# Optimization experiments

Hardware: AMD Instinct MI355X
Metric: run time of the kernel (lower is better)

Reference implementation:

```python
import jax, jax.numpy as jnp
import numpy as np
from jax.scipy.special import logsumexp

EPS = 1e-6
SINKHORN_ITERS = 8
TEMPERATURE = 1.0


def sinkhorn(logits):
    # log(clamp(t, min=eps)) / temperature, then alternating row/col log-normalization
    t = jnp.log(jnp.clip(logits, EPS)) / TEMPERATURE
    for _ in range(SINKHORN_ITERS):
        t = t - logsumexp(t, axis=-2, keepdims=True)  # over tokens n
        t = t - logsumexp(t, axis=-1, keepdims=True)  # over experts e
    return jnp.exp(t)


def setup_inputs() -> dict:
    key = jax.random.key(0)
    k1, k2, k3 = jax.random.split(key, 3)
    b, n, d, e, h = 4, 4096, 1024, 8, 1
    x = jax.random.normal(k1, (b, n, d), dtype=jnp.float32)
    gate_w = jax.random.normal(k2, (h, d, e), dtype=jnp.float32)  # to_gate_weight
    experts = jax.random.normal(k3, (e, d, d), dtype=jnp.float32) * 0.02  # expert weight tensor [e, i, o]
    return {"x": x, "gate_w": gate_w, "experts": experts}


def reference(x, gate_w, experts):
    b, n, d = x.shape
    h, _, e = gate_w.shape
    m = n // e  # tokens_per_expert

    xh = x[:, None]  # b 1 n d  (single-headed path)

    # gate logits: b h n e
    gate_logits = jnp.einsum('bhnd,hde->bhne', xh, gate_w)

    # competitive sinkhorn gates (eval mode, no gumbel noise)
    gates = sinkhorn(gate_logits)

    # topk over token dim (dim=-2) with k = tokens_per_expert
    g = jnp.swapaxes(gates, -1, -2)          # b h e n
    gv, idx = jax.lax.top_k(g, m)            # b h e m
    gate_values = jnp.swapaxes(gv, -1, -2)   # b h m e
    routed_indices = jnp.swapaxes(idx, -1, -2)  # b h m e

    # eval + competitive -> hard gates
    hard_gates = (gate_values > 0.5).astype(x.dtype)  # b h m e

    # gather routed tokens: routed[b,h,m,e,d] = x[b,h,idx[b,h,m,e],d]
    bi = jnp.arange(b)[:, None, None, None]
    hi = jnp.arange(h)[None, :, None, None]
    routed = xh[bi, hi, routed_indices]  # b h m e d

    # per-expert GEMM, vectorized over experts: experts [e,i,o] -> [e,h,i,o]
    experts4 = experts[:, None, :, :]
    out = jnp.einsum('bhmei,ehio->bhmeo', routed, experts4)  # b h m e o

    # weight by gates
    out = out * hard_gates[..., None]

    # scatter back (set semantics, as in einx set_at)
    y = jnp.zeros_like(xh).at[bi, hi, routed_indices].set(out)  # b h n d
    return y[:, 0]  # b n d
```

## Files before the change

### kernel.cpp

```cpp
#include <hip/hip_runtime.h>
#include <hip/hip_bf16.h>
#include <stdint.h>

#define BB 4
#define NN 4096
#define DD 1024
#define EE 8
#define MM 512
#define BN (BB*NN)

#define SBLK 32
#define SPB  8
#define SROWS 512

#define FRONT_GATE 512
#define FRONT_CONV 2048
#define FRONT_INIT 64
#define FRONT_BLKS (FRONT_GATE + FRONT_CONV + FRONT_INIT)

typedef __bf16 bf16x8 __attribute__((ext_vector_type(8)));
typedef float  floatx4 __attribute__((ext_vector_type(4)));

typedef const __attribute__((address_space(1))) void* gptr_t;
typedef __attribute__((address_space(3))) void* lptr_t;

__device__ __forceinline__ unsigned short f2bf(float f) {
    union { float f; unsigned u; } v; v.f = f;
    unsigned r = v.u + 0x7fffu + ((v.u >> 16) & 1u);
    return (unsigned short)(r >> 16);
}

__device__ __forceinline__ float gate_reduce8(const float acc[8], int lane) {
    float k1[4];
#pragma unroll
    for (int e = 0; e < 4; e++) {
        float a = acc[e]     + __shfl_xor(acc[e],     1, 64);
        float b = acc[e + 4] + __shfl_xor(acc[e + 4], 1, 64);
        k1[e] = (lane & 1) ? b : a;
    }
    float k2[2];
#pragma unroll
    for (int e = 0; e < 2; e++) {
        float a = k1[e]     + __shfl_xor(k1[e],     2, 64);
        float b = k1[e + 2] + __shfl_xor(k1[e + 2], 2, 64);
        k2[e] = (lane & 2) ? b : a;
    }
    float a = k2[0] + __shfl_xor(k2[0], 4, 64);
    float b = k2[1] + __shfl_xor(k2[1], 4, 64);
    float v = (lane & 4) ? b : a;
    v += __shfl_xor(v, 8, 64);
    v += __shfl_xor(v, 16, 64);
    v += __shfl_xor(v, 32, 64);
    return v;
}

#define OFF_GATES   0u
#define OFF_TOPK    524288u
#define OFF_WIN     589824u
#define OFF_COUNTS  655360u
#define OFF_LISTS   655616u
#define OFF_FLAGS   721152u
#define OFF_PART    737536u
#define OFF_KEYS    753920u
#define OFF_XBF     1802496u
#define OFF_EXPT    35356928u
#define WS_NEEDED   52134144u

__global__ __launch_bounds__(256, 2) void front_kernel(const float* __restrict__ x,
                                                       const float* __restrict__ gw,
                                                       const float* __restrict__ E,
                                                       float* __restrict__ tmat,
                                                       unsigned short* __restrict__ xbf,
                                                       unsigned short* __restrict__ expt,
                                                       int* __restrict__ win,
                                                       int* __restrict__ counts,
                                                       unsigned* __restrict__ flags) {
    __shared__ float tile[64][65];
    int bid = blockIdx.x;
    int tid = threadIdx.x;

    if (bid < FRONT_GATE) {
        int wave = tid >> 6, lane = tid & 63;
        float4 g0[4][4], g1[4][4];
#pragma unroll
        for (int j = 0; j < 4; j++)
#pragma unroll
            for (int r = 0; r < 4; r++) {
                const float4* p = (const float4*)(gw + (size_t)(j * 256 + lane * 4 + r) * 8);
                g0[j][r] = p[0];
                g1[j][r] = p[1];
            }
        int tok0 = (bid * 4 + wave) * 8;
        int exp_id = ((lane & 1) << 2) | (lane & 2) | ((lane & 4) >> 2);
        for (int tt = 0; tt < 8; tt += 2) {
            int tokA = tok0 + tt, tokB = tokA + 1;
            const float4* xrA = (const float4*)(x + (size_t)tokA * DD);
            const float4* xrB = (const float4*)(x + (size_t)tokB * DD);
            float4 xa[4], xc[4];
#pragma unroll
            for (int j = 0; j < 4; j++) xa[j] = xrA[j * 64 + lane];
#pragma unroll
            for (int j = 0; j < 4; j++) xc[j] = xrB[j * 64 + lane];
            if (xbf) {
#pragma unroll
                for (int j = 0; j < 4; j++) {
                    ushort4 o;
                    o.x = f2bf(xa[j].x); o.y = f2bf(xa[j].y); o.z = f2bf(xa[j].z); o.w = f2bf(xa[j].w);
                    ((ushort4*)(xbf + (size_t)tokA * DD))[j * 64 + lane] = o;
                }
#pragma unroll
                for (int j = 0; j < 4; j++) {
                    ushort4 o;
                    o.x = f2bf(xc[j].x); o.y = f2bf(xc[j].y); o.z = f2bf(xc[j].z); o.w = f2bf(xc[j].w);
                    ((ushort4*)(xbf + (size_t)tokB * DD))[j * 64 + lane] = o;
                }
            }
            float accA[8] = {0.f, 0.f, 0.f, 0.f, 0.f, 0.f, 0.f, 0.f};
            float accB[8] = {0.f, 0.f, 0.f, 0.f, 0.f, 0.f, 0.f, 0.f};
#pragma unroll
            for (int j = 0; j < 4; j++) {
                accA[0] += xa[j].x * g0[j][0].x + xa[j].y * g0[j][1].x + xa[j].z * g0[j][2].x + xa[j].w * g0[j][3].x;
                accA[1] += xa[j].x * g0[j][0].y + xa[j].y * g0[j][1].y + xa[j].z * g0[j][2].y + xa[j].w * g0[j][3].y;
                accA[2] += xa[j].x * g0[j][0].z + xa[j].y * g0[j][1].z + xa[j].z * g0[j][2].z + xa[j].w * g0[j][3].z;
                accA[3] += xa[j].x * g0[j][0].w + xa[j].y * g0[j][1].w + xa[j].z * g0[j][2].w + xa[j].w * g0[j][3].w;
                accA[4] += xa[j].x * g1[j][0].x + xa[j].y * g1[j][1].x + xa[j].z * g1[j][2].x + xa[j].w * g1[j][3].x;
                accA[5] += xa[j].x * g1[j][0].y + xa[j].y * g1[j][1].y + xa[j].z * g1[j][2].y + xa[j].w * g1[j][3].y;
                accA[6] += xa[j].x * g1[j][0].z + xa[j].y * g1[j][1].z + xa[j].z * g1[j][2].z + xa[j].w * g1[j][3].z;
                accA[7] += xa[j].x * g1[j][0].w + xa[j].y * g1[j][1].w + xa[j].z * g1[j][2].w + xa[j].w * g1[j][3].w;
                accB[0] += xc[j].x * g0[j][0].x + xc[j].y * g0[j][1].x + xc[j].z * g0[j][2].x + xc[j].w * g0[j][3].x;
                accB[1] += xc[j].x * g0[j][0].y + xc[j].y * g0[j][1].y + xc[j].z * g0[j][2].y + xc[j].w * g0[j][3].y;
                accB[2] += xc[j].x * g0[j][0].z + xc[j].y * g0[j][1].z + xc[j].z * g0[j][2].z + xc[j].w * g0[j][3].z;
                accB[3] += xc[j].x * g0[j][0].w + xc[j].y * g0[j][1].w + xc[j].z * g0[j][2].w + xc[j].w * g0[j][3].w;
                accB[4] += xc[j].x * g1[j][0].x + xc[j].y * g1[j][1].x + xc[j].z * g1[j][2].x + xc[j].w * g1[j][3].x;
                accB[5] += xc[j].x * g1[j][0].y + xc[j].y * g1[j][1].y + xc[j].z * g1[j][2].y + xc[j].w * g1[j][3].y;
                accB[6] += xc[j].x * g1[j][0].z + xc[j].y * g1[j][1].z + xc[j].z * g1[j][2].z + xc[j].w * g1[j][3].z;
                accB[7] += xc[j].x * g1[j][0].w + xc[j].y * g1[j][1].w + xc[j].z * g1[j][2].w + xc[j].w * g1[j][3].w;
            }
            float vA = gate_reduce8(accA, lane);
            float vB = gate_reduce8(accB, lane);
            if (lane < 8) {
                tmat[(size_t)tokA * EE + exp_id] = logf(fmaxf(vA, 1e-6f));
                tmat[(size_t)tokB * EE + exp_id] = logf(fmaxf(vB, 1e-6f));
            }
        }
    } else if (bid < FRONT_GATE + FRONT_CONV) {
        if (!expt) return;
        int cb = bid - FRONT_GATE;
        int e = cb >> 8, t = cb & 255;
        int k0 = (t >> 4) * 64, c0 = (t & 15) * 64;
#pragma unroll
        for (int ii = 0; ii < 4; ii++) {
            int r = (tid >> 4) + ii * 16;
            int c4 = (tid & 15) * 4;
            float4 v = *(const float4*)(E + ((size_t)e * DD + k0 + r) * DD + c0 + c4);
            tile[r][c4 + 0] = v.x; tile[r][c4 + 1] = v.y; tile[r][c4 + 2] = v.z; tile[r][c4 + 3] = v.w;
        }
        __syncthreads();
        int cc = tid >> 2, kk0 = (tid & 3) * 16;
#pragma unroll
        for (int q = 0; q < 4; q++) {
            ushort4 o;
            o.x = f2bf(tile[kk0 + q * 4 + 0][cc]);
            o.y = f2bf(tile[kk0 + q * 4 + 1][cc]);
            o.z = f2bf(tile[kk0 + q * 4 + 2][cc]);
            o.w = f2bf(tile[kk0 + q * 4 + 3][cc]);
            *(ushort4*)&expt[((size_t)e * DD + c0 + cc) * DD + k0 + kk0 + q * 4] = o;
        }
    } else {
        int i = (bid - FRONT_GATE - FRONT_CONV) * 256 + tid;
        win[i] = -1;
        if (i < 32) counts[i] = 0;
        if (i < 4096) flags[i] = 0u;
    }
}

__global__ __launch_bounds__(512) void sinkhorn_mb(const float* __restrict__ tmat,
                                                   float* __restrict__ part,
                                                   unsigned* __restrict__ flags,
                                                   unsigned long long* __restrict__ keys) {
    int g = blockIdx.x;
    int b = g >> 3, sl = g & 7;
    int tid = threadIdx.x;
    int wave = tid >> 6, lane = tid & 63;
    int row = sl * SROWS + tid;
    const float* tr = tmat + ((size_t)b * NN + row) * EE;
    float tv[EE];
#pragma unroll
    for (int e = 0; e < EE; e++) tv[e] = tr[e];

    __shared__ float red[8][8];
    __shared__ float bcm[8];

    for (int it = 0; it < 8; it++) {
#pragma unroll
        for (int e = 0; e < EE; e++) {
            float s = expf(tv[e]);
            for (int off = 32; off > 0; off >>= 1) s += __shfl_down(s, off, 64);
            if (lane == 0) red[wave][e] = s;
        }
        __syncthreads();
        if (tid == 0) {
            float* pm = part + (size_t)(it * 32 + b * 8 + sl) * 16;
#pragma unroll
            for (int e = 0; e < EE; e++) {
                float s = 0.f;
#pragma unroll
                for (int w = 0; w < 8; w++) s += red[w][e];
                __hip_atomic_store(&pm[e], s, __ATOMIC_RELAXED, __HIP_MEMORY_SCOPE_AGENT);
            }
            __hip_atomic_store(&flags[(size_t)(it * 32 + b * 8 + sl) * 16], 1u,
                               __ATOMIC_RELEASE, __HIP_MEMORY_SCOPE_AGENT);
        }
        if (tid < 8) {
            const unsigned* f = flags + (size_t)(it * 32 + b * 8 + tid) * 16;
            while (__hip_atomic_load(f, __ATOMIC_ACQUIRE, __HIP_MEMORY_SCOPE_AGENT) == 0u)
                __builtin_amdgcn_s_sleep(1);
        }
        __syncthreads();
        if (tid < 8) {
            const float* pb = part + (size_t)(it * 32 + b * 8) * 16;
            float s = 0.f;
#pragma unroll
            for (int p = 0; p < SPB; p++)
                s += __hip_atomic_load(&pb[p * 16 + tid], __ATOMIC_RELAXED, __HIP_MEMORY_SCOPE_AGENT);
            bcm[tid] = logf(s);
        }
        __syncthreads();
#pragma unroll
        for (int e = 0; e < EE; e++) tv[e] -= bcm[e];
        {
            float s = 0.f;
#pragma unroll
            for (int e = 0; e < EE; e++) s += expf(tv[e]);
            float lse = logf(s);
#pragma unroll
            for (int e = 0; e < EE; e++) tv[e] -= lse;
        }
    }
#pragma unroll
    for (int e = 0; e < EE; e++) {
        unsigned fb = __float_as_uint(expf(tv[e]));
        keys[(size_t)(b * EE + e) * NN + row] =
            ((unsigned long long)fb << 32) | (unsigned)(~row);
    }
}

__global__ __launch_bounds__(256) void rank_topk_kernel(const unsigned long long* __restrict__ keys,
                                                        float* __restrict__ topk_val,
                                                        int* __restrict__ win) {
    __shared__ unsigned long long K[NN];
    int be = blockIdx.y;
    int b = be >> 3, e = be & 7;
    int tid = threadIdx.x;
    const unsigned long long* kcol = keys + (size_t)be * NN;
    for (int i = tid; i < NN / 2; i += 256)
        ((ulonglong2*)K)[i] = ((const ulonglong2*)kcol)[i];
    __syncthreads();
    int t = blockIdx.x * 256 + tid;
    unsigned long long my = K[t];
    int cnt = 0;
    for (int j = 0; j < NN; j += 8) {
        ulonglong2 a = *(const ulonglong2*)&K[j + 0];
        ulonglong2 c = *(const ulonglong2*)&K[j + 2];
        ulonglong2 d = *(const ulonglong2*)&K[j + 4];
        ulonglong2 f = *(const ulonglong2*)&K[j + 6];
        cnt += (int)(a.x > my) + (int)(a.y > my) + (int)(c.x > my) + (int)(c.y > my)
             + (int)(d.x > my) + (int)(d.y > my) + (int)(f.x > my) + (int)(f.y > my);
    }
    if (cnt < MM) {
        topk_val[be * MM + cnt] = __uint_as_float((unsigned)(my >> 32));
        atomicMax(&win[b * NN + t], cnt * 8 + e);
    }
}

__global__ __launch_bounds__(256) void build_zero_kernel(const float* __restrict__ topk_val,
                                                         const int* __restrict__ win,
                                                         int* __restrict__ counts,
                                                         int* __restrict__ lists,
                                                         float* __restrict__ y) {
    __shared__ int act_s[64];
    int base = blockIdx.x * 64;
    int tid = threadIdx.x;
    if (tid < 64) {
        int i = base + tid;
        int b = i >> 12, tok = i & 4095;
        int w = win[i];
        int active = 0;
        if (w >= 0) {
            int m = w >> 3, e = w & 7;
            float gv = topk_val[(b * 8 + e) * MM + m];
            if (gv > 0.5f) {
                int p = atomicAdd(&counts[b * 8 + e], 1);
                lists[(b * 8 + e) * MM + p] = tok;
                active = 1;
            }
        }
        act_s[tid] = active;
    }
    __syncthreads();
    float4 z = make_float4(0.f, 0.f, 0.f, 0.f);
    for (int r = 0; r < 64; r++) {
        if (!act_s[r])
            ((float4*)(y + (size_t)(base + r) * DD))[tid] = z;
    }
}

__global__ __launch_bounds__(256) void expert_gemm_mfma(const unsigned short* __restrict__ xbf,
                                                        const unsigned short* __restrict__ expt,
                                                        const int* __restrict__ counts,
                                                        const int* __restrict__ lists,
                                                        float* __restrict__ y) {
    int be = blockIdx.z;
    int b = be >> 3, e = be & 7;
    int cnt = counts[be];
    int row0 = blockIdx.y * 64;
    if (row0 >= cnt) return;
    int col0 = blockIdx.x * 128;

    __shared__ unsigned short As[64 * 32];
    __shared__ unsigned short Bs[128 * 32];
    __shared__ int toks[64];

    int tid = threadIdx.x;
    int wave = tid >> 6, lane = tid & 63;
    int m16 = lane & 15, quad = lane >> 4;
    int wave_m = wave >> 1, wave_n = wave & 1;

    if (tid < 64) {
        int r = row0 + tid;
        toks[tid] = lists[be * MM + (r < cnt ? r : cnt - 1)];
    }

    int r0 = tid >> 2;
    int ch = tid & 3;

    const unsigned short* xb = xbf + (size_t)b * NN * DD;
    const unsigned short* Eb = expt + (size_t)e * DD * DD;

    floatx4 acc[2][4];
#pragma unroll
    for (int i = 0; i < 2; i++)
#pragma unroll
        for (int j = 0; j < 4; j++) acc[i][j] = (floatx4)0.f;

    for (int k0 = 0; k0 < DD; k0 += 32) {
        __syncthreads();
        {
            const unsigned short* gA  = xb + (size_t)toks[r0] * DD + k0 + ch * 8;
            const unsigned short* gB0 = Eb + (size_t)(col0 + r0) * DD + k0 + ch * 8;
            const unsigned short* gB1 = Eb + (size_t)(col0 + 64 + r0) * DD + k0 + ch * 8;
            __builtin_amdgcn_global_load_lds((gptr_t)gA,  (lptr_t)(As + (size_t)tid * 8), 16, 0, 0);
            __builtin_amdgcn_global_load_lds((gptr_t)gB0, (lptr_t)(Bs + (size_t)tid * 8), 16, 0, 0);
            __builtin_amdgcn_global_load_lds((gptr_t)gB1, (lptr_t)(Bs + 64 * 32 + (size_t)tid * 8), 16, 0, 0);
        }
        __syncthreads();
        bf16x8 af[2], bfr[4];
#pragma unroll
        for (int i = 0; i < 2; i++)
            af[i] = *(const bf16x8*)&As[(wave_m * 32 + i * 16 + m16) * 32 + quad * 8];
#pragma unroll
        for (int j = 0; j < 4; j++)
            bfr[j] = *(const bf16x8*)&Bs[(wave_n * 64 + j * 16 + m16) * 32 + quad * 8];
#pragma unroll
        for (int i = 0; i < 2; i++)
#pragma unroll
            for (int j = 0; j < 4; j++)
                acc[i][j] = __builtin_amdgcn_mfma_f32_16x16x32_bf16(af[i], bfr[j], acc[i][j], 0, 0, 0);
    }

#pragma unroll
    for (int i = 0; i < 2; i++) {
#pragma unroll
        for (int r = 0; r < 4; r++) {
            int lr = wave_m * 32 + i * 16 + quad * 4 + r;
            if (row0 + lr < cnt) {
                int tok = toks[lr];
                float* yr = y + ((size_t)b * NN + tok) * DD + col0 + wave_n * 64 + m16;
#pragma unroll
                for (int j = 0; j < 4; j++) yr[j * 16] = acc[i][j][r];
            }
        }
    }
}

__global__ __launch_bounds__(256) void expert_gemm_kernel(const float* __restrict__ x,
                                                          const float* __restrict__ experts,
                                                          const int* __restrict__ counts,
                                                          const int* __restrict__ lists,
                                                          float* __restrict__ y) {
    int be = blockIdx.z;
    int b = be >> 3, e = be & 7;
    int cnt = counts[be];
    int row0 = blockIdx.y * 64;
    if (row0 >= cnt) return;
    int col0 = blockIdx.x * 64;
    __shared__ float As2[16][68];
    __shared__ float Bs2[16][68];
    __shared__ int toks[64];
    int tid = threadIdx.x;
    if (tid < 64) {
        int r = row0 + tid;
        toks[tid] = (r < cnt) ? lists[be * MM + r] : -1;
    }
    __syncthreads();
    int tx = tid & 15, ty = tid >> 4;
    int ar = tid >> 2;
    int ak = (tid & 3) * 4;
    int bk = tid >> 4;
    int bc4 = (tid & 15) * 4;
    int atok = toks[ar];
    const float* xb = x + (size_t)b * NN * DD;
    const float* Eb = experts + (size_t)e * DD * DD + col0;
    float acc[4][4] = {};
    for (int k0 = 0; k0 < DD; k0 += 16) {
        float4 av;
        if (atok >= 0) av = *(const float4*)(xb + (size_t)atok * DD + k0 + ak);
        else av = make_float4(0.f, 0.f, 0.f, 0.f);
        float4 bv = *(const float4*)(Eb + (size_t)(k0 + bk) * DD + bc4);
        __syncthreads();
        As2[ak + 0][ar] = av.x; As2[ak + 1][ar] = av.y; As2[ak + 2][ar] = av.z; As2[ak + 3][ar] = av.w;
        *(float4*)&Bs2[bk][bc4] = bv;
        __syncthreads();
#pragma unroll
        for (int kk = 0; kk < 16; kk++) {
            float4 a = *(const float4*)&As2[kk][ty * 4];
            float4 bb = *(const float4*)&Bs2[kk][tx * 4];
            acc[0][0] += a.x * bb.x; acc[0][1] += a.x * bb.y; acc[0][2] += a.x * bb.z; acc[0][3] += a.x * bb.w;
            acc[1][0] += a.y * bb.x; acc[1][1] += a.y * bb.y; acc[1][2] += a.y * bb.z; acc[1][3] += a.y * bb.w;
            acc[2][0] += a.z * bb.x; acc[2][1] += a.z * bb.y; acc[2][2] += a.z * bb.z; acc[2][3] += a.z * bb.w;
            acc[3][0] += a.w * bb.x; acc[3][1] += a.w * bb.y; acc[3][2] += a.w * bb.z; acc[3][3] += a.w * bb.w;
        }
    }
#pragma unroll
    for (int i = 0; i < 4; i++) {
        int rl = ty * 4 + i;
        if (row0 + rl < cnt) {
            int tok = toks[rl];
            float4 o = make_float4(acc[i][0], acc[i][1], acc[i][2], acc[i][3]);
            *(float4*)(y + ((size_t)b * NN + tok) * DD + col0 + tx * 4) = o;
        }
    }
}

extern "C" void kernel_launch(void* const* d_in, const int* in_sizes, int n_in,
                              void* d_out, int out_size, void* d_ws, size_t ws_size,
                              hipStream_t stream) {
    const float* x       = (const float*)d_in[0];
    const float* gw      = (const float*)d_in[1];
    const float* experts = (const float*)d_in[2];
    float* y = (float*)d_out;

    char* ws = (char*)d_ws;
    float*    gates    = (float*)(ws + OFF_GATES);
    float*    topk_val = (float*)(ws + OFF_TOPK);
    int*      win      = (int*)(ws + OFF_WIN);
    int*      counts   = (int*)(ws + OFF_COUNTS);
    int*      lists    = (int*)(ws + OFF_LISTS);
    unsigned* flags    = (unsigned*)(ws + OFF_FLAGS);
    float*    part     = (float*)(ws + OFF_PART);
    unsigned long long* keys = (unsigned long long*)(ws + OFF_KEYS);
    bool big = ws_size >= WS_NEEDED;
    unsigned short* xbf  = big ? (unsigned short*)(ws + OFF_XBF)  : nullptr;
    unsigned short* expt = big ? (unsigned short*)(ws + OFF_EXPT) : nullptr;

    front_kernel<<<FRONT_BLKS, 256, 0, stream>>>(x, gw, experts, gates, xbf, expt,
                                                 win, counts, flags);
    sinkhorn_mb<<<SBLK, 512, 0, stream>>>(gates, part, flags, keys);
    rank_topk_kernel<<<dim3(16, 32), 256, 0, stream>>>(keys, topk_val, win);
    build_zero_kernel<<<256, 256, 0, stream>>>(topk_val, win, counts, lists, y);
    if (big)
        expert_gemm_mfma<<<dim3(8, 8, BB * EE), 256, 0, stream>>>(xbf, expt, counts, lists, y);
    else
        expert_gemm_kernel<<<dim3(16, 8, BB * EE), 256, 0, stream>>>(x, experts, counts, lists, y);
}
```

Before: 293.0 us.

## Rewrite top-k rank counting with register-resident keys and wave ballots

The rank kernel no longer stages a whole column of keys in shared memory and has each thread scan all 4096 entries. Each lane now keeps 64 keys in registers, and a wave ranks one candidate at a time by ballot-comparing the broadcast candidate against every key and popcounting the result. This removes the LDS traffic and bank pressure of the full scan, in exchange for high register use (64 u64 values per lane) and four candidates handled per step. Candidate keys are prefetched from global memory one group ahead.

```diff
diff --git a/kernel.cpp b/kernel.cpp
--- a/kernel.cpp
+++ b/kernel.cpp
@@ -245,32 +245,57 @@
     }
 }
 
-__global__ __launch_bounds__(256) void rank_topk_kernel(const unsigned long long* __restrict__ keys,
-                                                        float* __restrict__ topk_val,
-                                                        int* __restrict__ win) {
-    __shared__ unsigned long long K[NN];
+__global__ __launch_bounds__(256, 2) void rank_topk_kernel(const unsigned long long* __restrict__ keys,
+                                                           float* __restrict__ topk_val,
+                                                           int* __restrict__ win) {
     int be = blockIdx.y;
     int b = be >> 3, e = be & 7;
     int tid = threadIdx.x;
+    int lane = tid & 63;
+    int wave = __builtin_amdgcn_readfirstlane(tid >> 6);
     const unsigned long long* kcol = keys + (size_t)be * NN;
-    for (int i = tid; i < NN / 2; i += 256)
-        ((ulonglong2*)K)[i] = ((const ulonglong2*)kcol)[i];
-    __syncthreads();
-    int t = blockIdx.x * 256 + tid;
-    unsigned long long my = K[t];
-    int cnt = 0;
-    for (int j = 0; j < NN; j += 8) {
-        ulonglong2 a = *(const ulonglong2*)&K[j + 0];
-        ulonglong2 c = *(const ulonglong2*)&K[j + 2];
-        ulonglong2 d = *(const ulonglong2*)&K[j + 4];
-        ulonglong2 f = *(const ulonglong2*)&K[j + 6];
-        cnt += (int)(a.x > my) + (int)(a.y > my) + (int)(c.x > my) + (int)(c.y > my)
-             + (int)(d.x > my) + (int)(d.y > my) + (int)(f.x > my) + (int)(f.y > my);
-    }
-    if (cnt < MM) {
-        topk_val[be * MM + cnt] = __uint_as_float((unsigned)(my >> 32));
-        atomicMax(&win[b * NN + t], cnt * 8 + e);
-    }
+
+    ulonglong2 kj[32];
+#pragma unroll
+    for (int q = 0; q < 32; q++)
+        kj[q] = ((const ulonglong2*)kcol)[q * 64 + lane];
+
+    int t0 = (blockIdx.x * 4 + wave) * 64;
+
+#define TG 4
+    unsigned long long tk[TG];
+#pragma unroll
+    for (int i = 0; i < TG; i++) tk[i] = kcol[t0 + i];
+
+    for (int g = 0; g < 64 / TG; g++) {
+        int tbase = t0 + g * TG;
+        unsigned long long tn[TG];
+        if (g + 1 < 64 / TG) {
+#pragma unroll
+            for (int i = 0; i < TG; i++) tn[i] = kcol[tbase + TG + i];
+        }
+#pragma unroll
+        for (int i = 0; i < TG; i++) {
+            unsigned long long my = tk[i];
+            int cnt = 0;
+#pragma unroll
+            for (int q = 0; q < 32; q++) {
+                cnt += (int)__popcll(__ballot(kj[q].x > my));
+                cnt += (int)__popcll(__ballot(kj[q].y > my));
+            }
+            if (cnt < MM) {
+                if (lane == 0) {
+                    topk_val[be * MM + cnt] = __uint_as_float((unsigned)(my >> 32));
+                    atomicMax(&win[b * NN + tbase + i], cnt * 8 + e);
+                }
+            }
+        }
+        if (g + 1 < 64 / TG) {
+#pragma unroll
+            for (int i = 0; i < TG; i++) tk[i] = tn[i];
+        }
+    }
+#undef TG
 }
 
 __global__ __launch_bounds__(256) void build_zero_kernel(const float* __restrict__ topk_val,
```

New measurement: 296.7 us. Within noise of the previous version (+1.3%).
